# Kernel tuning notes

Hardware: AMD Instinct MI355X
Metric: run time of the kernel (lower is better)

Reference implementation:

```python
import jax, jax.numpy as jnp
import numpy as np

B, L = 1, 2048
D_MODEL, D_STATE, D_CONV, EXPAND = 512, 16, 4, 2
D_INNER = D_MODEL * EXPAND
EPS = 1e-10  # clamp used by the torch reference


def setup_inputs() -> dict:
    key = jax.random.key(0)
    ks = jax.random.split(key, 8)
    s = lambda fan: 1.0 / np.sqrt(fan)
    x = jax.random.normal(ks[0], (B, L, D_MODEL), jnp.float32)
    # Weights stored in (in, out) layout: y = x @ W  (equivalent to torch Linear with W.T)
    W_in = jax.random.normal(ks[1], (D_MODEL, 2 * D_INNER), jnp.float32) * s(D_MODEL)
    conv_w = jax.random.normal(ks[2], (D_INNER, 1, D_CONV), jnp.float32) * s(D_CONV)  # depthwise (O, I/groups, K)
    conv_b = jax.random.normal(ks[3], (D_INNER,), jnp.float32) * 0.01
    W_xproj = jax.random.normal(ks[4], (D_INNER, 2 * D_STATE + 1), jnp.float32) * s(D_INNER)
    dt_w = jax.random.normal(ks[5], (D_INNER,), jnp.float32) * 0.1  # Linear(1, d_inner) weight, squeezed
    dt_b = jax.random.normal(ks[6], (D_INNER,), jnp.float32) * 0.1 - 2.0  # keep delta smallish
    A_log = jnp.log(jnp.arange(1, D_STATE + 1, dtype=jnp.float32))
    D = jnp.ones((D_INNER,), jnp.float32)
    W_out = jax.random.normal(ks[7], (D_INNER, D_MODEL), jnp.float32) * s(D_INNER)
    return {"x": x, "W_in": W_in, "conv_w": conv_w, "conv_b": conv_b,
            "W_xproj": W_xproj, "dt_w": dt_w, "dt_b": dt_b,
            "A_log": A_log, "D": D, "W_out": W_out}


def reference(x, W_in, conv_w, conv_b, W_xproj, dt_w, dt_b, A_log, D, W_out):
    d_inner, _, d_conv = conv_w.shape
    d_state = A_log.shape[0]

    xz = x @ W_in                                    # (B, L, 2*d_inner)
    xs, z = jnp.split(xz, 2, axis=-1)

    # Depthwise causal conv1d: left-pad d_conv-1 == torch pad-both + truncate to L
    xc = jnp.transpose(xs, (0, 2, 1))                # (B, d_inner, L)
    xc = jax.lax.conv_general_dilated(
        xc, conv_w, window_strides=(1,), padding=[(d_conv - 1, 0)],
        feature_group_count=d_inner,
        dimension_numbers=("NCH", "OIH", "NCH")) + conv_b[None, :, None]
    xs = jax.nn.silu(jnp.transpose(xc, (0, 2, 1)))   # (B, L, d_inner)

    xp = xs @ W_xproj                                # (B, L, 2*d_state+1)
    delta = jax.nn.softplus(xp[..., 0:1] * dt_w + dt_b)  # (B, L, d_inner)
    Bp = xp[..., 1:1 + d_state]                      # (B, L, d_state)
    Cp = xp[..., 1 + d_state:]                       # (B, L, d_state)
    A = -jnp.exp(A_log)                              # (d_state,)

    # --- parallel selective scan via cumulative log-sum (faithful to source) ---
    A_bar = jnp.exp(delta[..., None] * A)                            # (B,L,Di,S)
    BX = delta[..., None] * Bp[:, :, None, :] * xs[..., None]        # (B,L,Di,S)
    log_A_bar = jnp.log(jnp.maximum(A_bar, EPS))
    A_cumsum = jnp.exp(jnp.cumsum(log_A_bar, axis=1))
    A_shift = jnp.concatenate([jnp.ones_like(A_cumsum[:, :1]), A_cumsum[:, :-1]], axis=1)
    weighted_BX = BX / jnp.maximum(A_shift, EPS)
    h = A_cumsum * jnp.cumsum(weighted_BX, axis=1) / jnp.maximum(A_bar, EPS)
    y = jnp.einsum("bls,blds->bld", Cp, h) + D * xs                  # (B,L,Di)

    y = y * jax.nn.silu(z)
    return y @ W_out                                                  # (B,L,D)
```

## Files before the change

### kernel.cpp

```cpp
#include <hip/hip_runtime.h>
#include <hip/hip_bf16.h>


#define L_SEQ 2048
#define DM 512
#define DI 1024
#define DS 16
#define NXP 33
#define EPS 1e-10f
#define RCPEPS 1e10f
#define LOG2E 1.44269504088896340736f
#define LN2 0.69314718055994530942f
#define LOG2EPS -33.219280948873623478f

typedef __hip_bfloat16 bf16;
typedef __attribute__((ext_vector_type(8))) short bf16x8v;
typedef __attribute__((ext_vector_type(4))) float f32x4v;
typedef __attribute__((ext_vector_type(4))) unsigned int u32x4v;

__device__ __forceinline__ float ldf(const float* p) { return *p; }
__device__ __forceinline__ float ldf(const bf16* p) { return __bfloat162float(*p); }

__device__ __forceinline__ void st1(float* p, float v) { *p = v; }
__device__ __forceinline__ void st1(bf16* p, float v) { *p = __float2bfloat16(v); }

__device__ __forceinline__ float fexp2(float x) { return __builtin_amdgcn_exp2f(x); }
__device__ __forceinline__ float frcp(float x) { return __builtin_amdgcn_rcpf(x); }

__device__ __forceinline__ void load8(const float* p, float* v) {
  float4 a = *(const float4*)p;
  float4 b = *(const float4*)(p + 4);
  v[0] = a.x; v[1] = a.y; v[2] = a.z; v[3] = a.w;
  v[4] = b.x; v[5] = b.y; v[6] = b.z; v[7] = b.w;
}
__device__ __forceinline__ void load8(const bf16* p, float* v) {
  bf16 t[8];
  *(uint4*)t = *(const uint4*)p;
#pragma unroll
  for (int j = 0; j < 8; ++j) v[j] = __bfloat162float(t[j]);
}

__global__ __launch_bounds__(256)
void transpose_cast_kernel(const float* __restrict__ W, bf16* __restrict__ WT,
                           int R, int C) {
  __shared__ float tile[32][33];
  int c0 = blockIdx.x * 32, r0 = blockIdx.y * 32;
  int tx = threadIdx.x & 31, ty = threadIdx.x >> 5;
#pragma unroll
  for (int i = 0; i < 4; ++i) {
    int rr = ty + i * 8;
    tile[rr][tx] = W[(size_t)(r0 + rr) * C + c0 + tx];
  }
  __syncthreads();
#pragma unroll
  for (int i = 0; i < 4; ++i) {
    int cc = ty + i * 8;
    WT[(size_t)(c0 + cc) * R + r0 + tx] = __float2bfloat16(tile[tx][cc]);
  }
}

template <typename TA, typename TC>
__global__ __launch_bounds__(256)
void gemm_bt64(const TA* __restrict__ A, const bf16* __restrict__ BT,
               TC* __restrict__ C, int M, int N, int K, int lda, int ldc) {
  __shared__ __align__(16) bf16 As[64 * 40];
  __shared__ __align__(16) bf16 Bs[64 * 40];
  const int tid = threadIdx.x;
  const int wave = tid >> 6, lane = tid & 63;
  const int q = lane >> 4, r = lane & 15;
  const int row0 = blockIdx.y * 64, col0 = blockIdx.x * 64;
  const int srow = tid >> 2, sseg = tid & 3;
  f32x4v acc[4] = {};
  for (int k0 = 0; k0 < K; k0 += 32) {
    {
      float v[8];
      load8(A + (size_t)(row0 + srow) * lda + k0 + sseg * 8, v);
      bf16* dst = &As[srow * 40 + sseg * 8];
#pragma unroll
      for (int j = 0; j < 8; ++j) dst[j] = __float2bfloat16(v[j]);
    }
    *(uint4*)&Bs[srow * 40 + sseg * 8] =
        *(const uint4*)(BT + (size_t)(col0 + srow) * K + k0 + sseg * 8);
    __syncthreads();
    bf16x8v a = *(const bf16x8v*)&As[(wave * 16 + r) * 40 + q * 8];
#pragma unroll
    for (int j = 0; j < 4; ++j) {
      bf16x8v b = *(const bf16x8v*)&Bs[(j * 16 + r) * 40 + q * 8];
      acc[j] = __builtin_amdgcn_mfma_f32_16x16x32_bf16(a, b, acc[j], 0, 0, 0);
    }
    __syncthreads();
  }
#pragma unroll
  for (int j = 0; j < 4; ++j)
#pragma unroll
    for (int reg = 0; reg < 4; ++reg) {
      int m = row0 + wave * 16 + q * 4 + reg;
      int n = col0 + j * 16 + r;
      st1(C + (size_t)m * ldc + n, acc[j][reg]);
    }
}

template <>
__global__ __launch_bounds__(256)
void gemm_bt64<bf16, float>(const bf16* __restrict__ A, const bf16* __restrict__ BT,
                            float* __restrict__ C, int M, int N, int K,
                            int lda, int ldc) {
  __shared__ __align__(16) bf16 As[64 * 40];
  __shared__ __align__(16) bf16 Bs[64 * 40];
  const int tid = threadIdx.x;
  const int wave = tid >> 6, lane = tid & 63;
  const int q = lane >> 4, r = lane & 15;
  const int row0 = blockIdx.y * 64, col0 = blockIdx.x * 64;
  const int srow = tid >> 2, sseg = tid & 3;
  f32x4v acc[4] = {};
  for (int k0 = 0; k0 < K; k0 += 32) {
    *(uint4*)&As[srow * 40 + sseg * 8] =
        *(const uint4*)(A + (size_t)(row0 + srow) * lda + k0 + sseg * 8);
    *(uint4*)&Bs[srow * 40 + sseg * 8] =
        *(const uint4*)(BT + (size_t)(col0 + srow) * K + k0 + sseg * 8);
    __syncthreads();
    bf16x8v a = *(const bf16x8v*)&As[(wave * 16 + r) * 40 + q * 8];
#pragma unroll
    for (int j = 0; j < 4; ++j) {
      bf16x8v b = *(const bf16x8v*)&Bs[(j * 16 + r) * 40 + q * 8];
      acc[j] = __builtin_amdgcn_mfma_f32_16x16x32_bf16(a, b, acc[j], 0, 0, 0);
    }
    __syncthreads();
  }
#pragma unroll
  for (int j = 0; j < 4; ++j)
#pragma unroll
    for (int reg = 0; reg < 4; ++reg) {
      int m = row0 + wave * 16 + q * 4 + reg;
      int n = col0 + j * 16 + r;
      st1(C + (size_t)m * ldc + n, acc[j][reg]);
    }
}

__global__ __launch_bounds__(256)
void gemm_xproj(const bf16* __restrict__ A, const float* __restrict__ Wx,
                float* __restrict__ xpcT) {
  __shared__ __align__(16) bf16 As[64 * 40];
  __shared__ __align__(16) bf16 Bs[64 * 40];
  const int tid = threadIdx.x;
  const int wave = tid >> 6, lane = tid & 63;
  const int q = lane >> 4, r = lane & 15;
  const int row0 = blockIdx.y * 64;
  const int srow = tid >> 2, sseg = tid & 3;
  f32x4v acc[4] = {};
  for (int k0 = 0; k0 < DI; k0 += 32) {
    *(uint4*)&As[srow * 40 + sseg * 8] =
        *(const uint4*)(A + (size_t)(row0 + srow) * DI + k0 + sseg * 8);
    int k = tid >> 3, n0 = (tid & 7) * 8;
#pragma unroll
    for (int j = 0; j < 8; ++j) {
      int n = n0 + j;
      float v = (n < NXP) ? Wx[(size_t)(k0 + k) * NXP + n] : 0.f;
      Bs[n * 40 + k] = __float2bfloat16(v);
    }
    __syncthreads();
    bf16x8v a = *(const bf16x8v*)&As[(wave * 16 + r) * 40 + q * 8];
#pragma unroll
    for (int j = 0; j < 4; ++j) {
      bf16x8v b = *(const bf16x8v*)&Bs[(j * 16 + r) * 40 + q * 8];
      acc[j] = __builtin_amdgcn_mfma_f32_16x16x32_bf16(a, b, acc[j], 0, 0, 0);
    }
    __syncthreads();
  }
#pragma unroll
  for (int j = 0; j < 4; ++j)
#pragma unroll
    for (int reg = 0; reg < 4; ++reg) {
      int m = row0 + wave * 16 + q * 4 + reg;
      int n = j * 16 + r;
      if (n < NXP) xpcT[(size_t)n * L_SEQ + m] = acc[j][reg];
    }
}

__global__ __launch_bounds__(256)
void conv_silu_dual(const bf16* __restrict__ xz, const float* __restrict__ conv_w,
                    const float* __restrict__ conv_b, bf16* __restrict__ xs,
                    bf16* __restrict__ xsT) {
  __shared__ bf16 tile[67][72];
  __shared__ bf16 sout[64][72];
  const int tid = threadIdx.x;
  const int d0 = blockIdx.x * 64, l0 = blockIdx.y * 64;
  for (int slot = tid; slot < 67 * 8; slot += 256) {
    int rr = slot >> 3, seg = slot & 7;
    int l = l0 - 3 + rr;
    uint4 v = {0, 0, 0, 0};
    if (l >= 0) v = *(const uint4*)(xz + (size_t)l * (2 * DI) + d0 + seg * 8);
    *(uint4*)&tile[rr][seg * 8] = v;
  }
  __syncthreads();
  {
    int lr = tid >> 3, c0t = (tid & 7) * 8;
#pragma unroll
    for (int half = 0; half < 2; ++half) {
      int lrow = lr + half * 32;
      bf16 o[8];
#pragma unroll
      for (int j = 0; j < 8; ++j) {
        int c = c0t + j;
        float acc = conv_b[d0 + c];
#pragma unroll
        for (int k = 0; k < 4; ++k)
          acc = fmaf(__bfloat162float(tile[lrow + k][c]), conv_w[(d0 + c) * 4 + k], acc);
        float v = acc / (1.f + __expf(-acc));
        o[j] = __float2bfloat16(v);
        sout[c][lrow] = o[j];
      }
      *(uint4*)(xs + (size_t)(l0 + lrow) * DI + d0 + c0t) = *(uint4*)o;
    }
  }
  __syncthreads();
  for (int slot = tid; slot < 64 * 8; slot += 256) {
    int dd = slot >> 3, seg = slot & 7;
    *(uint4*)(xsT + (size_t)(d0 + dd) * L_SEQ + l0 + seg * 8) =
        *(uint4*)&sout[dd][seg * 8];
  }
}

__global__ __launch_bounds__(256)
void gate_transpose_kernel(const bf16* __restrict__ yT, const bf16* __restrict__ zbuf,
                           int ldz, bf16* __restrict__ ys) {
  __shared__ bf16 tile[64][72];
  int d0 = blockIdx.y * 64, l0 = blockIdx.x * 64;
#pragma unroll
  for (int it = 0; it < 2; ++it) {
    int slot = threadIdx.x + it * 256;
    int dd = slot >> 3, seg = slot & 7;
    *(uint4*)&tile[dd][seg * 8] = *(const uint4*)(yT + (size_t)(d0 + dd) * L_SEQ + l0 + seg * 8);
  }
  __syncthreads();
#pragma unroll
  for (int it = 0; it < 2; ++it) {
    int slot = threadIdx.x + it * 256;
    int ll = slot >> 3, seg = slot & 7;
    bf16 zt[8];
    *(uint4*)zt = *(const uint4*)(zbuf + (size_t)(l0 + ll) * ldz + d0 + seg * 8);
    bf16 o[8];
#pragma unroll
    for (int j = 0; j < 8; ++j) {
      float yv = __bfloat162float(tile[seg * 8 + j][ll]);
      float zv = __bfloat162float(zt[j]);
      o[j] = __float2bfloat16(yv * zv * frcp(1.f + fexp2(-zv * LOG2E)));
    }
    *(uint4*)(ys + (size_t)(l0 + ll) * DI + d0 + seg * 8) = *(uint4*)o;
  }
}

#define LC 512
#define NW 16
#define SPW 32
#define PSX 513
#define LCP 516

__global__ __launch_bounds__(1024)
void scan_kernel(bf16* __restrict__ xsT, const float* __restrict__ xpcT,
                 const float* __restrict__ dt_w, const float* __restrict__ dt_b,
                 const float* __restrict__ A_log, const float* __restrict__ Dvec) {
  __shared__ float sxpT[NXP * PSX];
  __shared__ float sdt[4 * LCP], sg[4 * LCP], sxs[4 * LCP];
  __shared__ float sys[4 * LCP];
  __shared__ float Wtot[NW][64], Vtot[NW][64];
  const int tid = threadIdx.x;
  const int wave = tid >> 6, lane = tid & 63;
  const int s = lane & 15, dl = lane >> 4;
  const int d0 = blockIdx.x * 4;
  const int base = wave * SPW;
  const float As2 = -expf(A_log[s]) * LOG2E;
  const float Dd = Dvec[d0 + dl];
  float dtw[4], dtb[4];
#pragma unroll
  for (int c = 0; c < 4; ++c) {
    dtw[c] = dt_w[d0 + c];
    dtb[c] = dt_b[d0 + c];
  }
  float cs2_carry = 0.f, S_carry = 0.f;
  for (int l0 = 0; l0 < L_SEQ; l0 += LC) {
    for (int idx = tid; idx < NXP * LC; idx += 1024) {
      int j = idx >> 9, l = idx & (LC - 1);
      sxpT[j * PSX + l] = xpcT[(size_t)j * L_SEQ + l0 + l];
    }
    for (int slot = tid; slot < 4 * (LC / 8); slot += 1024) {
      int c = slot >> 6, seg = slot & 63;
      bf16 tmp[8];
      *(uint4*)tmp = *(const uint4*)(xsT + (size_t)(d0 + c) * L_SEQ + l0 + seg * 8);
#pragma unroll
      for (int j = 0; j < 8; ++j) sxs[c * LCP + seg * 8 + j] = __bfloat162float(tmp[j]);
    }
    __syncthreads();
    for (int i = tid; i < LC; i += 1024) {
      float x0 = sxpT[i];
#pragma unroll
      for (int c = 0; c < 4; ++c) {
        float a = fmaf(x0, dtw[c], dtb[c]);
        float dt = __log2f(1.f + fexp2(a * LOG2E)) * LN2;
        sdt[c * LCP + i] = dt;
        sg[c * LCP + i] = dt * sxs[c * LCP + i];
      }
    }
    __syncthreads();
    float P[SPW];
    float Wl = 0.f;
#pragma unroll
    for (int k = 0; k < SPW; ++k) {
      float u = sdt[dl * LCP + base + k] * As2;
      P[k] = Wl;
      Wl += fmaxf(u, LOG2EPS);
    }
    Wtot[wave][lane] = Wl;
    __syncthreads();
    float O = cs2_carry, Wall = 0.f;
    for (int w = 0; w < NW; ++w) {
      float t = Wtot[w][lane];
      if (w < wave) O += t;
      Wall += t;
    }
    float Vl = 0.f;
#pragma unroll
    for (int k = 0; k < SPW; ++k) {
      float rcpA = fminf(fexp2(-(O + P[k])), RCPEPS);
      float gb = sg[dl * LCP + base + k] * sxpT[(1 + s) * PSX + base + k];
      Vl = fmaf(gb, rcpA, Vl);
    }
    Vtot[wave][lane] = Vl;
    __syncthreads();
    float SO = S_carry, Vall = 0.f;
    for (int w = 0; w < NW; ++w) {
      float t = Vtot[w][lane];
      if (w < wave) SO += t;
      Vall += t;
    }
    float S = SO;
#pragma unroll
    for (int k = 0; k < SPW; ++k) {
      float xk = O + P[k];
      float rcpA = fminf(fexp2(-xk), RCPEPS);
      float aprev = fexp2(xk);
      float gb = sg[dl * LCP + base + k] * sxpT[(1 + s) * PSX + base + k];
      S = fmaf(gb, rcpA, S);
      float h = aprev * S;
      float contrib = sxpT[(17 + s) * PSX + base + k] * h;
      contrib += __shfl_xor(contrib, 8);
      contrib += __shfl_xor(contrib, 4);
      contrib += __shfl_xor(contrib, 2);
      contrib += __shfl_xor(contrib, 1);
      if (s == 0)
        sys[dl * LCP + base + k] = contrib + Dd * sxs[dl * LCP + base + k];
    }
    cs2_carry += Wall;
    S_carry += Vall;
    __syncthreads();
    for (int slot = tid; slot < 4 * (LC / 8); slot += 1024) {
      int c = slot >> 6, seg = slot & 63;
      bf16 tmp[8];
#pragma unroll
      for (int j = 0; j < 8; ++j) tmp[j] = __float2bfloat16(sys[c * LCP + seg * 8 + j]);
      u32x4v vv;
      vv.x = ((unsigned int*)tmp)[0]; vv.y = ((unsigned int*)tmp)[1];
      vv.z = ((unsigned int*)tmp)[2]; vv.w = ((unsigned int*)tmp)[3];
      __builtin_nontemporal_store(vv,
          (u32x4v*)(xsT + (size_t)(d0 + c) * L_SEQ + l0 + seg * 8));
    }
    __syncthreads();
  }
}

extern "C" void kernel_launch(void* const* d_in, const int* in_sizes, int n_in,
                              void* d_out, int out_size, void* d_ws, size_t ws_size,
                              hipStream_t stream) {
  const float* x       = (const float*)d_in[0];
  const float* W_in    = (const float*)d_in[1];
  const float* conv_w  = (const float*)d_in[2];
  const float* conv_b  = (const float*)d_in[3];
  const float* W_xproj = (const float*)d_in[4];
  const float* dt_w    = (const float*)d_in[5];
  const float* dt_b    = (const float*)d_in[6];
  const float* A_log   = (const float*)d_in[7];
  const float* Dvec    = (const float*)d_in[8];
  const float* W_out   = (const float*)d_in[9];
  float* out = (float*)d_out;

  char* ws = (char*)d_ws;
  const size_t MB = 1024 * 1024;
  bf16* xz    = (bf16*)(ws);
  bf16* buf1  = (bf16*)(ws + 8 * MB);
  bf16* WinT  = (bf16*)(ws + 12 * MB);
  bf16* xsT   = (bf16*)(ws + 12 * MB);
  bf16* WoutT = (bf16*)(ws + 12 * MB);
  float* xpcT = (float*)(ws + 16 * MB);

  transpose_cast_kernel<<<dim3(2 * DI / 32, DM / 32), 256, 0, stream>>>(
      W_in, WinT, DM, 2 * DI);
  gemm_bt64<float, bf16><<<dim3(2 * DI / 64, L_SEQ / 64), 256, 0, stream>>>(
      x, WinT, xz, L_SEQ, 2 * DI, DM, DM, 2 * DI);
  conv_silu_dual<<<dim3(DI / 64, L_SEQ / 64), 256, 0, stream>>>(
      xz, conv_w, conv_b, buf1, xsT);
  gemm_xproj<<<dim3(1, L_SEQ / 64), 256, 0, stream>>>(buf1, W_xproj, xpcT);
  scan_kernel<<<DI / 4, 1024, 0, stream>>>(xsT, xpcT, dt_w, dt_b, A_log, Dvec);
  gate_transpose_kernel<<<dim3(L_SEQ / 64, DI / 64), 256, 0, stream>>>(
      xsT, xz + DI, 2 * DI, buf1);
  transpose_cast_kernel<<<dim3(DM / 32, DI / 32), 256, 0, stream>>>(
      W_out, WoutT, DI, DM);
  gemm_bt64<bf16, float><<<dim3(DM / 64, L_SEQ / 64), 256, 0, stream>>>(
      buf1, WoutT, out, L_SEQ, DM, DI, DI, DM);
}
```

Baseline: 215.8 us.

## Defer scan output stores into next chunk, vectorize loads, cache scan terms

Moves each chunk's bf16 write-back of the scan output to the top of the next chunk iteration, which removes one barrier per chunk and lets the stores overlap the next chunk's loads. A final flush handles the last chunk. The xp staging load becomes float4-vectorized, with the shared-memory pitch padded to 516 so rows stay 16-byte aligned. The delta/softplus loop is spread over all 4x512 elements so every thread does work, and the per-step gb*rcpA terms are kept in registers instead of being recomputed, saving one exp2 and the shared loads per step at the cost of more registers.

```diff
diff --git a/kernel.cpp b/kernel.cpp
--- a/kernel.cpp
+++ b/kernel.cpp
@@ -253,7 +253,7 @@
 #define LC 512
 #define NW 16
 #define SPW 32
-#define PSX 513
+#define PSX 516
 #define LCP 516
 
 __global__ __launch_bounds__(1024)
@@ -279,9 +279,24 @@
   }
   float cs2_carry = 0.f, S_carry = 0.f;
   for (int l0 = 0; l0 < L_SEQ; l0 += LC) {
-    for (int idx = tid; idx < NXP * LC; idx += 1024) {
-      int j = idx >> 9, l = idx & (LC - 1);
-      sxpT[j * PSX + l] = xpcT[(size_t)j * L_SEQ + l0 + l];
+    if (l0) {
+      int lp = l0 - LC;
+      for (int slot = tid; slot < 4 * (LC / 8); slot += 1024) {
+        int c = slot >> 6, seg = slot & 63;
+        bf16 tmp[8];
+#pragma unroll
+        for (int j = 0; j < 8; ++j) tmp[j] = __float2bfloat16(sys[c * LCP + seg * 8 + j]);
+        u32x4v vv;
+        vv.x = ((unsigned int*)tmp)[0]; vv.y = ((unsigned int*)tmp)[1];
+        vv.z = ((unsigned int*)tmp)[2]; vv.w = ((unsigned int*)tmp)[3];
+        __builtin_nontemporal_store(vv,
+            (u32x4v*)(xsT + (size_t)(d0 + c) * L_SEQ + lp + seg * 8));
+      }
+    }
+    for (int idx = tid; idx < NXP * (LC / 4); idx += 1024) {
+      int j = idx >> 7, l4 = idx & 127;
+      *(float4*)&sxpT[j * PSX + l4 * 4] =
+          *(const float4*)(xpcT + (size_t)j * L_SEQ + l0 + l4 * 4);
     }
     for (int slot = tid; slot < 4 * (LC / 8); slot += 1024) {
       int c = slot >> 6, seg = slot & 63;
@@ -291,15 +306,13 @@
       for (int j = 0; j < 8; ++j) sxs[c * LCP + seg * 8 + j] = __bfloat162float(tmp[j]);
     }
     __syncthreads();
-    for (int i = tid; i < LC; i += 1024) {
+    for (int idx = tid; idx < 4 * LC; idx += 1024) {
+      int c = idx >> 9, i = idx & (LC - 1);
       float x0 = sxpT[i];
-#pragma unroll
-      for (int c = 0; c < 4; ++c) {
-        float a = fmaf(x0, dtw[c], dtb[c]);
-        float dt = __log2f(1.f + fexp2(a * LOG2E)) * LN2;
-        sdt[c * LCP + i] = dt;
-        sg[c * LCP + i] = dt * sxs[c * LCP + i];
-      }
+      float a = fmaf(x0, dtw[c], dtb[c]);
+      float dt = __log2f(1.f + fexp2(a * LOG2E)) * LN2;
+      sdt[c * LCP + i] = dt;
+      sg[c * LCP + i] = dt * sxs[c * LCP + i];
     }
     __syncthreads();
     float P[SPW];
@@ -318,30 +331,28 @@
       if (w < wave) O += t;
       Wall += t;
     }
+    float t[SPW];
     float Vl = 0.f;
 #pragma unroll
     for (int k = 0; k < SPW; ++k) {
       float rcpA = fminf(fexp2(-(O + P[k])), RCPEPS);
       float gb = sg[dl * LCP + base + k] * sxpT[(1 + s) * PSX + base + k];
-      Vl = fmaf(gb, rcpA, Vl);
+      t[k] = gb * rcpA;
+      Vl += t[k];
     }
     Vtot[wave][lane] = Vl;
     __syncthreads();
     float SO = S_carry, Vall = 0.f;
     for (int w = 0; w < NW; ++w) {
-      float t = Vtot[w][lane];
-      if (w < wave) SO += t;
-      Vall += t;
+      float tv = Vtot[w][lane];
+      if (w < wave) SO += tv;
+      Vall += tv;
     }
     float S = SO;
 #pragma unroll
     for (int k = 0; k < SPW; ++k) {
-      float xk = O + P[k];
-      float rcpA = fminf(fexp2(-xk), RCPEPS);
-      float aprev = fexp2(xk);
-      float gb = sg[dl * LCP + base + k] * sxpT[(1 + s) * PSX + base + k];
-      S = fmaf(gb, rcpA, S);
-      float h = aprev * S;
+      S += t[k];
+      float h = fexp2(O + P[k]) * S;
       float contrib = sxpT[(17 + s) * PSX + base + k] * h;
       contrib += __shfl_xor(contrib, 8);
       contrib += __shfl_xor(contrib, 4);
@@ -353,6 +364,9 @@
     cs2_carry += Wall;
     S_carry += Vall;
     __syncthreads();
+  }
+  {
+    int lp = L_SEQ - LC;
     for (int slot = tid; slot < 4 * (LC / 8); slot += 1024) {
       int c = slot >> 6, seg = slot & 63;
       bf16 tmp[8];
@@ -362,9 +376,8 @@
       vv.x = ((unsigned int*)tmp)[0]; vv.y = ((unsigned int*)tmp)[1];
       vv.z = ((unsigned int*)tmp)[2]; vv.w = ((unsigned int*)tmp)[3];
       __builtin_nontemporal_store(vv,
-          (u32x4v*)(xsT + (size_t)(d0 + c) * L_SEQ + l0 + seg * 8));
-    }
-    __syncthreads();
+          (u32x4v*)(xsT + (size_t)(d0 + c) * L_SEQ + lp + seg * 8));
+    }
   }
 }
 
```

After: 226.0 us. +4.7%, slower.
